# Kernel optimization log

Hardware: AMD Instinct MI355X
Metric: run time of the kernel (lower is better)

## Reference

```python
import jax, jax.numpy as jnp
import numpy as np

B, S, D, E = 4, 2048, 2048, 8


def setup_inputs() -> dict:
    key = jax.random.key(0)
    ks = jax.random.split(key, 5)
    scale = 1.0 / np.sqrt(D)
    x = jax.random.normal(ks[0], (B, S, D), dtype=jnp.float32)
    # experts: torch Linear stores W as [out, in]; y = x @ W.T + b
    expert_w = jax.random.uniform(ks[1], (E, D, D), dtype=jnp.float32, minval=-scale, maxval=scale)
    expert_b = jax.random.uniform(ks[2], (E, D), dtype=jnp.float32, minval=-scale, maxval=scale)
    router_w = jax.random.uniform(ks[3], (E, D), dtype=jnp.float32, minval=-scale, maxval=scale)
    router_b = jax.random.uniform(ks[4], (E,), dtype=jnp.float32, minval=-scale, maxval=scale)
    return {"x": x, "expert_w": expert_w, "expert_b": expert_b,
            "router_w": router_w, "router_b": router_b}


def reference(x, expert_w, expert_b, router_w, router_b):
    b, s, d = x.shape
    n_exp = expert_w.shape[0]
    xf = x.reshape(b * s, d)                       # [N, D]
    logits = xf @ router_w.T + router_b            # [N, E]
    probs = jax.nn.softmax(logits, axis=-1)
    expert_id = jnp.argmax(probs, axis=-1)         # [N] top-1 routing
    top_prob = jnp.max(probs, axis=-1)             # [N] gate weight
    out = jnp.zeros_like(xf)
    # dense-equivalent of the masked gather/scatter: each expert's linear
    # applied to all tokens, masked by routing decision (E is small & static)
    for i in range(n_exp):
        y = xf @ expert_w[i].T + expert_b[i]       # [N, D]
        out = out + jnp.where((expert_id == i)[:, None], y, 0.0)
    out = out * top_prob[:, None]
    # forward never calls compute_loss; returns loss = 0
    return out.reshape(b, s, d), jnp.float32(0.0)
```

## Files before the change

### kernel.cpp

```cpp
#include <hip/hip_runtime.h>
#include <hip/hip_bf16.h>

#define N_TOK 8192
#define DIM   2048
#define NEXP  8
#define BM    288
#define BN    256
#define BK    32
#define NT    (DIM / BK)
#define NBLK  256

#define A_BYTES  (BM * BK * 2)
#define B_BYTES  (BN * BK * 2)
#define RING     (A_BYTES + B_BYTES)
#define DYN_LDS  (4 * RING)

typedef __attribute__((ext_vector_type(8))) short  short8;
typedef __attribute__((ext_vector_type(4))) float  f32x4;
typedef __attribute__((ext_vector_type(4))) unsigned int u32x4;

static __device__ __forceinline__ unsigned int pack_bf2(float a, float b) {
  union { __hip_bfloat16 h; unsigned short u; } ca, cb;
  ca.h = __float2bfloat16(a);
  cb.h = __float2bfloat16(b);
  return ((unsigned int)cb.u << 16) | (unsigned int)ca.u;
}

static __device__ __forceinline__ void gload16(const unsigned short* g, void* l) {
  __builtin_amdgcn_global_load_lds(
      (const __attribute__((address_space(1))) unsigned int*)(const void*)g,
      (__attribute__((address_space(3))) unsigned int*)l, 16, 0, 0);
}

static __device__ __forceinline__ double dot8d(const float4& x0, const float4& x1,
                                               const float4& w0, const float4& w1) {
  double a = 0.0;
  a = fma((double)x0.x, (double)w0.x, a);
  a = fma((double)x0.y, (double)w0.y, a);
  a = fma((double)x0.z, (double)w0.z, a);
  a = fma((double)x0.w, (double)w0.w, a);
  a = fma((double)x1.x, (double)w1.x, a);
  a = fma((double)x1.y, (double)w1.y, a);
  a = fma((double)x1.z, (double)w1.z, a);
  a = fma((double)x1.w, (double)w1.w, a);
  return a;
}

__global__ __launch_bounds__(256) void convw_kernel(
    const float* __restrict__ w, unsigned short* __restrict__ wbuf)
{
  const size_t c0 = (size_t)blockIdx.x * 1024 + threadIdx.x;
  float4 f[8];
#pragma unroll
  for (int i = 0; i < 4; i++) {
    const float4* s = reinterpret_cast<const float4*>(w + (c0 + i * 256) * 8);
    f[2 * i]     = s[0];
    f[2 * i + 1] = s[1];
  }
#pragma unroll
  for (int i = 0; i < 4; i++) {
    u32x4 pk;
    pk[0] = pack_bf2(f[2*i].x,   f[2*i].y);   pk[1] = pack_bf2(f[2*i].z,   f[2*i].w);
    pk[2] = pack_bf2(f[2*i+1].x, f[2*i+1].y); pk[3] = pack_bf2(f[2*i+1].z, f[2*i+1].w);
    *reinterpret_cast<u32x4*>(wbuf + (c0 + i * 256) * 8) = pk;
  }
}

__global__ __launch_bounds__(256, 3) void router_kernel(
    const float* __restrict__ x, const float* __restrict__ rw,
    const float* __restrict__ rb, int* __restrict__ eid,
    float* __restrict__ gate, unsigned short* __restrict__ xb)
{
  const int t    = threadIdx.x;
  const int tok0 = blockIdx.x * 4;

  float4 w0[NEXP], w1[NEXP];
#pragma unroll
  for (int e = 0; e < NEXP; e++) {
    const float4* wr = reinterpret_cast<const float4*>(rw + (size_t)e * DIM);
    w0[e] = wr[2 * t];
    w1[e] = wr[2 * t + 1];
  }
  float4 xv0[4], xv1[4];
#pragma unroll
  for (int k = 0; k < 4; k++) {
    const float4* xr = reinterpret_cast<const float4*>(x + (size_t)(tok0 + k) * DIM);
    xv0[k] = xr[2 * t];
    xv1[k] = xr[2 * t + 1];
  }
#pragma unroll
  for (int k = 0; k < 4; k++) {
    u32x4 pk;
    pk[0] = pack_bf2(xv0[k].x, xv0[k].y); pk[1] = pack_bf2(xv0[k].z, xv0[k].w);
    pk[2] = pack_bf2(xv1[k].x, xv1[k].y); pk[3] = pack_bf2(xv1[k].z, xv1[k].w);
    *reinterpret_cast<u32x4*>(xb + (size_t)(tok0 + k) * DIM + t * 8) = pk;
  }

  __shared__ double red[4][4][NEXP];
  const int lane = t & 63, wv = t >> 6;
#pragma unroll
  for (int k = 0; k < 4; k++) {
    double s[NEXP];
#pragma unroll
    for (int e = 0; e < NEXP; e++) s[e] = dot8d(xv0[k], xv1[k], w0[e], w1[e]);
#pragma unroll
    for (int e = 0; e < NEXP; e++) {
      double v = s[e];
#pragma unroll
      for (int off = 32; off > 0; off >>= 1) v += __shfl_xor(v, off, 64);
      if (lane == 0) red[wv][k][e] = v;
    }
  }
  __syncthreads();
  if (t < 4) {
    double lg[NEXP];
    double lmax = -1e300; int best = 0;
#pragma unroll
    for (int e = 0; e < NEXP; e++) {
      lg[e] = red[0][t][e] + red[1][t][e] + red[2][t][e] + red[3][t][e] + (double)rb[e];
      if (lg[e] > lmax) { lmax = lg[e]; best = e; }
    }
    float den = 0.f;
#pragma unroll
    for (int e = 0; e < NEXP; e++) den += expf((float)(lg[e] - lmax));
    eid[tok0 + t]  = best;
    gate[tok0 + t] = 1.0f / den;
  }
}

__global__ __launch_bounds__(1024) void histo_perm(
    const int* __restrict__ eid, int* __restrict__ counts, int* __restrict__ perm)
{
  __shared__ int hist[NEXP], baseS[NEXP], fillS[NEXP];
  const int t = threadIdx.x;
  if (t < NEXP) { hist[t] = 0; fillS[t] = 0; }
  __syncthreads();
  int my[8];
#pragma unroll
  for (int i = 0; i < 8; i++) {
    my[i] = eid[t + i * 1024];
    atomicAdd(&hist[my[i]], 1);
  }
  __syncthreads();
  if (t == 0) {
    int b = 0;
#pragma unroll
    for (int e = 0; e < NEXP; e++) { counts[e] = hist[e]; baseS[e] = b; b += hist[e]; }
  }
  __syncthreads();
#pragma unroll
  for (int i = 0; i < 8; i++) {
    int pos = baseS[my[i]] + atomicAdd(&fillS[my[i]], 1);
    perm[pos] = t + i * 1024;
  }
}

__global__ __launch_bounds__(512, 2) void moe_gemm(
    const unsigned short* __restrict__ xb, const unsigned short* __restrict__ wb,
    const float* __restrict__ eb, const float* __restrict__ gate,
    const int* __restrict__ perm, const int* __restrict__ counts,
    float* __restrict__ out)
{
  extern __shared__ char smem[];
  __shared__ int   aRowS[BM];
  __shared__ float gateS[BM];

  const int tid  = threadIdx.x;
  const int lane = tid & 63, wid = tid >> 6;

  int ttot = 0;
#pragma unroll
  for (int j = 0; j < NEXP; j++) ttot += (counts[j] + BM - 1) / BM;
  ttot *= 8;

  const int nA5 = (wid < 2);
  int aR0[3], bR0[2];
  aR0[0] = (wid * 2) * 16;
  aR0[1] = (wid * 2 + 1) * 16;
  aR0[2] = nA5 ? ((16 + wid) * 16) : aR0[0];
  bR0[0] = (wid * 2) * 16;
  bR0[1] = (wid * 2 + 1) * 16;
  int aDst[3], bDst[2];
#pragma unroll
  for (int i = 0; i < 3; i++) aDst[i] = aR0[i] * 64;
#pragma unroll
  for (int i = 0; i < 2; i++) bDst[i] = A_BYTES + bR0[i] * 64;
  const int lrow = lane >> 2;
  const int cblk = (lane & 3) ^ ((lane >> 3) & 3);

  const int l15 = lane & 15;
  const int wr = wid >> 2, wc = wid & 3;
  const int sw   = (((lane >> 4) ^ ((l15 >> 1) & 3)) * 16);
  const int aOff = (wr * 144 + l15) * 64 + sw;
  const int bOff = A_BYTES + (wc * 64 + l15) * 64 + sw;
  const int rsub = (lane >> 4) * 4;

  for (int tt = blockIdx.x; tt < ttot; tt += NBLK) {
    const int bx = tt >> 3, by = tt & 7;

    int e = 0, rowbase = 0, nrows = 0, found = 0;
    {
      int tsum = 0, bsum = 0;
#pragma unroll
      for (int j = 0; j < NEXP; j++) {
        int cj = counts[j];
        int te = (cj + BM - 1) / BM;
        if (!found && bx < tsum + te) {
          int loc = bx - tsum;
          e = j;
          rowbase = bsum + loc * BM;
          int rem = cj - loc * BM;
          nrows = rem < BM ? rem : BM;
          found = 1;
        }
        tsum += te; bsum += cj;
      }
    }

    __syncthreads();
    if (tid < BM) {
      int idx = tid < nrows ? tid : (nrows - 1);
      int tok = perm[rowbase + idx];
      aRowS[tid] = tok;
      gateS[tid] = gate[tok];
    }
    __syncthreads();

    const unsigned short* wB = wb + (size_t)e * DIM * DIM;
    const unsigned short* aSrc[3];
    const unsigned short* bSrc[2];
#pragma unroll
    for (int i = 0; i < 3; i++)
      aSrc[i] = xb + (size_t)aRowS[aR0[i] + lrow] * DIM + cblk * 8;
#pragma unroll
    for (int i = 0; i < 2; i++)
      bSrc[i] = wB + (size_t)(by * BN + bR0[i] + lrow) * DIM + cblk * 8;

#pragma unroll
    for (int p = 0; p < 3; p++) {
      char* base = smem + p * RING;
      gload16(aSrc[0], base + aDst[0]);
      gload16(aSrc[1], base + aDst[1]);
      if (nA5) gload16(aSrc[2], base + aDst[2]);
      gload16(bSrc[0], base + bDst[0]);
      gload16(bSrc[1], base + bDst[1]);
      aSrc[0] += BK; aSrc[1] += BK; aSrc[2] += BK;
      bSrc[0] += BK; bSrc[1] += BK;
    }

    f32x4 acc[9][4] = {};

#pragma unroll 1
    for (int t = 0; t < NT; ++t) {
      if (t < NT - 2) {
        if (nA5) asm volatile("s_waitcnt vmcnt(10)" ::: "memory");
        else     asm volatile("s_waitcnt vmcnt(8)"  ::: "memory");
      } else if (t == NT - 2) {
        if (nA5) asm volatile("s_waitcnt vmcnt(5)" ::: "memory");
        else     asm volatile("s_waitcnt vmcnt(4)" ::: "memory");
      } else {
        asm volatile("s_waitcnt vmcnt(0)" ::: "memory");
      }
      __builtin_amdgcn_s_barrier();

      if (t + 3 < NT) {
        char* base = smem + ((t + 3) & 3) * RING;
        gload16(aSrc[0], base + aDst[0]);
        gload16(aSrc[1], base + aDst[1]);
        if (nA5) gload16(aSrc[2], base + aDst[2]);
        gload16(bSrc[0], base + bDst[0]);
        gload16(bSrc[1], base + bDst[1]);
        aSrc[0] += BK; aSrc[1] += BK; aSrc[2] += BK;
        bSrc[0] += BK; bSrc[1] += BK;
      }

      const char* cur = smem + (t & 3) * RING;
      short8 af[9], bf[4];
#pragma unroll
      for (int n = 0; n < 4; n++) bf[n] = *(const short8*)(cur + bOff + n * 1024);
#pragma unroll
      for (int m = 0; m < 9; m++) af[m] = *(const short8*)(cur + aOff + m * 1024);
      __builtin_amdgcn_s_setprio(1);
#pragma unroll
      for (int m = 0; m < 9; m++)
#pragma unroll
        for (int n = 0; n < 4; n++)
          acc[m][n] = __builtin_amdgcn_mfma_f32_16x16x32_bf16(af[m], bf[n], acc[m][n], 0, 0, 0);
      __builtin_amdgcn_s_setprio(0);
    }

    const int cb = by * BN + wc * 64;
    const float* ebE = eb + (size_t)e * DIM;
    float bias[4];
#pragma unroll
    for (int n = 0; n < 4; n++) bias[n] = ebE[cb + n * 16 + l15];
#pragma unroll
    for (int m = 0; m < 9; m++) {
      int r0 = wr * 144 + m * 16 + rsub;
#pragma unroll
      for (int rg = 0; rg < 4; rg++) {
        int r = r0 + rg;
        if (r < nrows) {
          float g = gateS[r];
          float* orow = out + (size_t)aRowS[r] * DIM + cb;
#pragma unroll
          for (int n = 0; n < 4; n++)
            orow[n * 16 + l15] = (acc[m][n][rg] + bias[n]) * g;
        }
      }
    }
    asm volatile("s_waitcnt vmcnt(0)" ::: "memory");
  }
}

extern "C" void kernel_launch(void* const* d_in, const int* in_sizes, int n_in,
                              void* d_out, int out_size, void* d_ws, size_t ws_size,
                              hipStream_t stream)
{
  const float* x  = (const float*)d_in[0];
  const float* ew = (const float*)d_in[1];
  const float* eb = (const float*)d_in[2];
  const float* rw = (const float*)d_in[3];
  const float* rb = (const float*)d_in[4];
  float* out = (float*)d_out;

  char* ws = (char*)d_ws;
  int*   eid    = (int*)(ws);
  float* gate   = (float*)(ws + 32 * 1024);
  int*   counts = (int*)(ws + 64 * 1024);
  int*   perm   = (int*)(ws + 128 * 1024);
  unsigned short* xbuf = (unsigned short*)(ws + 192 * 1024);
  unsigned short* wbuf = (unsigned short*)(ws + 192 * 1024 + ((size_t)N_TOK * DIM * 2));

  hipFuncSetAttribute(reinterpret_cast<const void*>(moe_gemm),
                      hipFuncAttributeMaxDynamicSharedMemorySize, DYN_LDS);

  hipMemsetAsync(out + (size_t)N_TOK * DIM, 0, sizeof(float), stream);
  convw_kernel<<<4096, 256, 0, stream>>>(ew, wbuf);
  router_kernel<<<N_TOK / 4, 256, 0, stream>>>(x, rw, rb, eid, gate, xbuf);
  histo_perm<<<1, 1024, 0, stream>>>(eid, counts, perm);
  moe_gemm<<<NBLK, 512, DYN_LDS, stream>>>(xbuf, wbuf, eb, gate, perm, counts, out);
}
```

Measured before the change: 176.2 us.

## Double-buffer LDS fragment registers to overlap LDS reads with MFMA

Restructures the GEMM main loop into a software pipeline with two register fragment sets. Each step now reads the next K-slice from LDS while the MFMAs consume the previously loaded fragments. The loop is unrolled by four with fixed ring-slot pointers, and the wait and barrier placement is adjusted to match. The goal is to hide LDS read latency behind matrix math. The cost is roughly doubled fragment register usage, which raises register pressure and the risk of spills.

```diff
diff --git a/kernel.cpp b/kernel.cpp
--- a/kernel.cpp
+++ b/kernel.cpp
@@ -155,6 +155,50 @@
   }
 }
 
+#define VMW(N) asm volatile("s_waitcnt vmcnt(" #N ")" ::: "memory")
+#define BARM() asm volatile("s_barrier" ::: "memory")
+
+#define GLOADS(GS)                                                          \
+  do {                                                                      \
+    gload16(aSrc[0], (GS) + aDst[0]);                                       \
+    gload16(aSrc[1], (GS) + aDst[1]);                                       \
+    if (nA5) gload16(aSrc[2], (GS) + aDst[2]);                              \
+    gload16(bSrc[0], (GS) + bDst[0]);                                       \
+    gload16(bSrc[1], (GS) + bDst[1]);                                       \
+    aSrc[0] += BK; aSrc[1] += BK; aSrc[2] += BK;                            \
+    bSrc[0] += BK; bSrc[1] += BK;                                           \
+  } while (0)
+
+#define DS_READS(RS, RAF, RBF)                                              \
+  do {                                                                      \
+    _Pragma("unroll")                                                       \
+    for (int n = 0; n < 4; n++) RBF[n] = *(const short8*)((RS) + bOff + n * 1024); \
+    _Pragma("unroll")                                                       \
+    for (int m = 0; m < 9; m++) RAF[m] = *(const short8*)((RS) + aOff + m * 1024); \
+  } while (0)
+
+#define MFMA36(MAF, MBF)                                                    \
+  do {                                                                      \
+    __builtin_amdgcn_sched_barrier(0);                                      \
+    __builtin_amdgcn_s_setprio(1);                                          \
+    _Pragma("unroll")                                                       \
+    for (int m = 0; m < 9; m++)                                             \
+      _Pragma("unroll")                                                     \
+      for (int n = 0; n < 4; n++)                                           \
+        acc[m][n] = __builtin_amdgcn_mfma_f32_16x16x32_bf16(MAF[m], MBF[n], \
+                                                            acc[m][n], 0, 0, 0); \
+    __builtin_amdgcn_s_setprio(0);                                          \
+  } while (0)
+
+#define STEP(RS, RAF, RBF, MAF, MBF, GS)                                    \
+  do {                                                                      \
+    if (nA5) VMW(5); else VMW(4);                                           \
+    BARM();                                                                 \
+    GLOADS(GS);                                                             \
+    DS_READS(RS, RAF, RBF);                                                 \
+    MFMA36(MAF, MBF);                                                       \
+  } while (0)
+
 __global__ __launch_bounds__(512, 2) void moe_gemm(
     const unsigned short* __restrict__ xb, const unsigned short* __restrict__ wb,
     const float* __restrict__ eb, const float* __restrict__ gate,
@@ -194,6 +238,11 @@
   const int aOff = (wr * 144 + l15) * 64 + sw;
   const int bOff = A_BYTES + (wc * 64 + l15) * 64 + sw;
   const int rsub = (lane >> 4) * 4;
+
+  char* const s0 = smem;
+  char* const s1 = smem + RING;
+  char* const s2 = smem + 2 * RING;
+  char* const s3 = smem + 3 * RING;
 
   for (int tt = blockIdx.x; tt < ttot; tt += NBLK) {
     const int bx = tt >> 3, by = tt & 7;
@@ -236,58 +285,35 @@
     for (int i = 0; i < 2; i++)
       bSrc[i] = wB + (size_t)(by * BN + bR0[i] + lrow) * DIM + cblk * 8;
 
-#pragma unroll
-    for (int p = 0; p < 3; p++) {
-      char* base = smem + p * RING;
-      gload16(aSrc[0], base + aDst[0]);
-      gload16(aSrc[1], base + aDst[1]);
-      if (nA5) gload16(aSrc[2], base + aDst[2]);
-      gload16(bSrc[0], base + bDst[0]);
-      gload16(bSrc[1], base + bDst[1]);
-      aSrc[0] += BK; aSrc[1] += BK; aSrc[2] += BK;
-      bSrc[0] += BK; bSrc[1] += BK;
-    }
+    GLOADS(s0); GLOADS(s1); GLOADS(s2);
+    if (nA5) VMW(10); else VMW(8);
+    BARM();
 
     f32x4 acc[9][4] = {};
+    short8 afA[9], bfA[4], afB[9], bfB[4];
+    DS_READS(s0, afA, bfA);
 
 #pragma unroll 1
-    for (int t = 0; t < NT; ++t) {
-      if (t < NT - 2) {
-        if (nA5) asm volatile("s_waitcnt vmcnt(10)" ::: "memory");
-        else     asm volatile("s_waitcnt vmcnt(8)"  ::: "memory");
-      } else if (t == NT - 2) {
-        if (nA5) asm volatile("s_waitcnt vmcnt(5)" ::: "memory");
-        else     asm volatile("s_waitcnt vmcnt(4)" ::: "memory");
-      } else {
-        asm volatile("s_waitcnt vmcnt(0)" ::: "memory");
-      }
-      __builtin_amdgcn_s_barrier();
-
-      if (t + 3 < NT) {
-        char* base = smem + ((t + 3) & 3) * RING;
-        gload16(aSrc[0], base + aDst[0]);
-        gload16(aSrc[1], base + aDst[1]);
-        if (nA5) gload16(aSrc[2], base + aDst[2]);
-        gload16(bSrc[0], base + bDst[0]);
-        gload16(bSrc[1], base + bDst[1]);
-        aSrc[0] += BK; aSrc[1] += BK; aSrc[2] += BK;
-        bSrc[0] += BK; bSrc[1] += BK;
-      }
-
-      const char* cur = smem + (t & 3) * RING;
-      short8 af[9], bf[4];
-#pragma unroll
-      for (int n = 0; n < 4; n++) bf[n] = *(const short8*)(cur + bOff + n * 1024);
-#pragma unroll
-      for (int m = 0; m < 9; m++) af[m] = *(const short8*)(cur + aOff + m * 1024);
-      __builtin_amdgcn_s_setprio(1);
-#pragma unroll
-      for (int m = 0; m < 9; m++)
-#pragma unroll
-        for (int n = 0; n < 4; n++)
-          acc[m][n] = __builtin_amdgcn_mfma_f32_16x16x32_bf16(af[m], bf[n], acc[m][n], 0, 0, 0);
-      __builtin_amdgcn_s_setprio(0);
-    }
+    for (int k = 0; k < 15; ++k) {
+      STEP(s1, afB, bfB, afA, bfA, s3);
+      STEP(s2, afA, bfA, afB, bfB, s0);
+      STEP(s3, afB, bfB, afA, bfA, s1);
+      STEP(s0, afA, bfA, afB, bfB, s2);
+    }
+    STEP(s1, afB, bfB, afA, bfA, s3);
+    {
+      if (nA5) VMW(5); else VMW(4);
+      BARM();
+      DS_READS(s2, afA, bfA);
+      MFMA36(afB, bfB);
+    }
+    {
+      VMW(0);
+      BARM();
+      DS_READS(s3, afB, bfB);
+      MFMA36(afA, bfA);
+    }
+    MFMA36(afB, bfB);
 
     const int cb = by * BN + wc * 64;
     const float* ebE = eb + (size_t)e * DIM;
@@ -309,7 +335,7 @@
         }
       }
     }
-    asm volatile("s_waitcnt vmcnt(0)" ::: "memory");
+    VMW(0);
   }
 }
 
```

Measured after the change: 379.8 us. +115.5%, slower.
